# Kernel optimization log

Hardware: AMD Instinct MI355X
Metric: run time of the kernel (lower is better)

The kernel has to match this reference:

```python
import math
import jax, jax.numpy as jnp
import numpy as np

T, B, E, H = 2048, 1, 2048, 32
HD = E // H          # head_dim = 64
HALF = HD // 2       # rotary half = 32
SCALE_LENGTH = 1024


def duplicate_interleave(m):
    # [S, HALF] -> [S, HD], each column duplicated adjacently
    return jnp.repeat(m, 2, axis=-1)


def rotate_every_two(x):
    # x: [BH, S, HD]
    x1 = x[:, :, ::2]
    x2 = x[:, :, 1::2]
    return jnp.stack((-x2, x1), axis=-1).reshape(x.shape)


def apply_rotary_pos_emb(x, sin, cos, scale):
    # sin/cos/scale: [S, HALF]; x: [BH, S, HD]
    sin2 = duplicate_interleave(sin * scale)
    cos2 = duplicate_interleave(cos * scale)
    return x * cos2 + rotate_every_two(x) * sin2


def setup_inputs() -> dict:
    key = jax.random.key(0)
    ks = jax.random.split(key, 8)
    std = 0.02
    query = jax.random.normal(ks[0], (T, B, E), jnp.float32)
    key_t = jax.random.normal(ks[1], (T, B, E), jnp.float32)
    value = jax.random.normal(ks[2], (T, B, E), jnp.float32)
    Wq = jax.random.normal(ks[3], (E, E), jnp.float32) * std
    Wk = jax.random.normal(ks[4], (E, E), jnp.float32) * std
    Wv = jax.random.normal(ks[5], (E, E), jnp.float32) * std
    Wo = jax.random.normal(ks[6], (E, E), jnp.float32) * std
    bq = jnp.zeros((E,), jnp.float32)
    bk = jnp.zeros((E,), jnp.float32)
    bv = jnp.zeros((E,), jnp.float32)
    bo = jnp.zeros((E,), jnp.float32)
    # XPos-style rotary tables
    pos = jnp.arange(T, dtype=jnp.float32)
    inv_freq = 1.0 / (10000.0 ** (jnp.arange(HALF, dtype=jnp.float32) / HALF))
    ang = pos[:, None] * inv_freq[None, :]          # [T, HALF]
    sin = jnp.sin(ang)
    cos = jnp.cos(ang)
    scale_base = 512.0
    dim_scale = (jnp.arange(0, HD, 2, dtype=jnp.float32) + 0.4 * HD) / (1.4 * HD)
    xscale = dim_scale[None, :] ** (pos[:, None] / scale_base)  # [T, HALF]
    # causal additive mask
    attn_mask = jnp.where(jnp.triu(jnp.ones((T, T), bool), k=1), -1e9, 0.0).astype(jnp.float32)
    return {"query": query, "key": key_t, "value": value,
            "Wq": Wq, "bq": bq, "Wk": Wk, "bk": bk, "Wv": Wv, "bv": bv,
            "Wo": Wo, "bo": bo, "sin": sin, "cos": cos, "xscale": xscale,
            "attn_mask": attn_mask, "scale_length": SCALE_LENGTH}


def reference(query, key, value, Wq, bq, Wk, bk, Wv, bv, Wo, bo,
              sin, cos, xscale, attn_mask, scale_length):
    tgt_len, bsz, embed_dim = query.shape
    scaling = HD ** -0.5

    def proj(x, W, b):
        y = x @ W.T + b                                # [T, B, E]
        return y.reshape(tgt_len, bsz * H, HD).transpose(1, 0, 2)  # [BH, T, HD]

    q = proj(query, Wq, bq)
    k = proj(key, Wk, bk)
    v = proj(value, Wv, bv)

    # self-attention XPos rotary: k scaled by 1/xscale, q by xscale (last q_len rows)
    k = apply_rotary_pos_emb(k, sin, cos, 1.0 / xscale)
    q = apply_rotary_pos_emb(q, sin[-tgt_len:], cos[-tgt_len:], xscale[-tgt_len:])

    src_len = k.shape[1]
    if src_len > scale_length:
        pos_k = jnp.arange(src_len - tgt_len, src_len, dtype=jnp.float32)
        scale_attention = jnp.maximum(1.0, jnp.log(pos_k) / math.log(scale_length))
        q = q * scale_attention[None, :, None]

    q = q * scaling
    attn_weights = jnp.einsum('btd,bsd->bts', q, k)      # [BH, T, S]
    attn_weights = attn_weights + attn_mask[None, :, :]
    attn_weights = jax.nn.softmax(attn_weights.astype(jnp.float32), axis=-1
                                  ).astype(q.dtype)
    attn = jnp.einsum('bts,bsd->btd', attn_weights, v)   # [BH, T, HD]
    attn = attn.transpose(1, 0, 2).reshape(tgt_len, bsz, embed_dim)
    attn = attn @ Wo.T + bo
    return attn
```

## Files before the change

### kernel.cpp

```cpp
#include <hip/hip_runtime.h>
#include <hip/hip_bf16.h>
#include <math.h>

#define T_LEN 2048
#define EMB   2048
#define NH    32
#define HD    64
#define HALF  32

typedef __attribute__((ext_vector_type(8))) short short8v;
typedef __attribute__((ext_vector_type(4))) float floatx4;

__device__ inline void gload_lds16(const void* g, void* l) {
    __builtin_amdgcn_global_load_lds(
        (const __attribute__((address_space(1))) unsigned int*)g,
        (__attribute__((address_space(3))) unsigned int*)l,
        16, 0, 0);
}

__device__ inline ushort f2bf(float x) {
    union { float f; unsigned u; } c; c.f = x;
    const unsigned r = c.u + 0x7FFFu + ((c.u >> 16) & 1u);
    return (ushort)(r >> 16);
}

#define BARRIER() do { asm volatile("" ::: "memory"); \
    __builtin_amdgcn_s_barrier(); asm volatile("" ::: "memory"); } while (0)
#define VMW8() asm volatile("s_waitcnt vmcnt(8)" ::: "memory")
#define VMW0() asm volatile("s_waitcnt vmcnt(0)" ::: "memory")

__global__ __launch_bounds__(256) void conv_all(
    const float* __restrict__ s0, const float* __restrict__ s1,
    const float* __restrict__ s2, const float* __restrict__ s3,
    const float* __restrict__ s4, const float* __restrict__ s5,
    const float* __restrict__ s6, ushort* __restrict__ dst,
    const float* __restrict__ sinp, const float* __restrict__ cosp,
    const float* __restrict__ xscale,
    float2* __restrict__ qt, float2* __restrict__ kt)
{
    if (blockIdx.x >= 14336) {
        const int idx = (blockIdx.x - 14336) * 256 + threadIdx.x;
        const int t = idx >> 5;
        const float s = sinp[idx], c = cosp[idx], xs = xscale[idx];
        float sa = 1.f;
        if (t >= 2) {
            const float lv = __logf((float)t) * 0.14426950408889634f;
            sa = lv > 1.f ? lv : 1.f;
        }
        const float qs = xs * sa * 0.125f * 1.4426950408889634f;
        qt[idx] = make_float2(c * qs, s * qs);
        const float ks = 1.f / xs;
        kt[idx] = make_float2(c * ks, s * ks);
        return;
    }
    const int idx = blockIdx.x * 256 + threadIdx.x;
    const int t = idx >> 19;
    const int r = (idx & 524287) * 8;
    const float* in = t == 0 ? s0 : t == 1 ? s1 : t == 2 ? s2 : t == 3 ? s3
                    : t == 4 ? s4 : t == 5 ? s5 : s6;
    const float4 v0 = *reinterpret_cast<const float4*>(&in[r]);
    const float4 v1 = *reinterpret_cast<const float4*>(&in[r + 4]);
    ushort o[8];
    o[0] = f2bf(v0.x); o[1] = f2bf(v0.y); o[2] = f2bf(v0.z); o[3] = f2bf(v0.w);
    o[4] = f2bf(v1.x); o[5] = f2bf(v1.y); o[6] = f2bf(v1.z); o[7] = f2bf(v1.w);
    *reinterpret_cast<uint4*>(&dst[(size_t)t * 4194304 + r]) =
        *reinterpret_cast<const uint4*>(o);
}

#define QBM 256
#define QBN 256

#define STAGE_A3(tau, h, slot) do {                                            \
    const int _tc = (tau) * 64;                                                \
    _Pragma("unroll") for (int _i = 0; _i < 2; ++_i) {                         \
        gload_lds16(&Ap[(size_t)(bm + (h) * 128 + wid * 16 + _i * 8 + rl) * 2048 + _tc + csw], \
                    &lds[(slot) * 16384 + (h) * 8192 + (wid * 16 + _i * 8) * 64]); \
    } } while (0)

#define STAGE_B2(tau, h, slot) do {                                            \
    const int _tc = (tau) * 64;                                                \
    _Pragma("unroll") for (int _i = 0; _i < 2; ++_i) {                         \
        gload_lds16(&Bp[(size_t)(bn + (h) * 128 + wid * 16 + _i * 8 + rl) * 2048 + _tc + csw], \
                    &lds[49152 + (slot) * 16384 + (h) * 8192 + (wid * 16 + _i * 8) * 64]); \
    } } while (0)

#define PH(sa_, sb_, mp, VMWSTMT, ...) do {                                    \
    if ((mp) == 0) {                                                           \
        _Pragma("unroll") for (int n = 0; n < 4; ++n) {                        \
            bf[n][0] = ldB(sb_, n, 0);                                         \
            bf[n][1] = ldB(sb_, n, 1);                                         \
        }                                                                      \
    }                                                                          \
    af[0][0] = ldA(sa_, (mp) * 2, 0);     af[0][1] = ldA(sa_, (mp) * 2, 1);    \
    af[1][0] = ldA(sa_, (mp) * 2 + 1, 0); af[1][1] = ldA(sa_, (mp) * 2 + 1, 1);\
    __VA_ARGS__;                                                               \
    BARRIER();                                                                 \
    __builtin_amdgcn_s_setprio(1);                                             \
    _Pragma("unroll") for (int mm = 0; mm < 2; ++mm)                           \
    _Pragma("unroll") for (int n = 0; n < 4; ++n)                              \
    _Pragma("unroll") for (int kk = 0; kk < 2; ++kk)                           \
        acc[(mp) * 2 + mm][n] = __builtin_amdgcn_mfma_f32_16x16x32_bf16(       \
            af[mm][kk], bf[n][kk], acc[(mp) * 2 + mm][n], 0, 0, 0);            \
    __builtin_amdgcn_s_setprio(0);                                             \
    VMWSTMT;                                                                   \
    BARRIER();                                                                 \
} while (0)

#define TILE6(sa, sb, sa2, tau2, LASTVMW) do {                                 \
    PH(sa, sb, 0, (void)0, STAGE_A3(tau2, 0, sa2));                            \
    PH(sa, sb, 1, (void)0, STAGE_A3(tau2, 1, sa2));                            \
    PH(sa, sb, 2, (void)0, STAGE_B2(tau2, 0, sb));                             \
    PH(sa, sb, 3, LASTVMW, STAGE_B2(tau2, 1, sb));                             \
} while (0)

__global__ __launch_bounds__(512, 2) void gemm_qkv8(
    const ushort* __restrict__ Astack,
    const ushort* __restrict__ Wstack,
    const float* __restrict__ bq, const float* __restrict__ bk,
    const float* __restrict__ bv,
    ushort* __restrict__ outQ, ushort* __restrict__ outK,
    ushort* __restrict__ outVt,
    const float2* __restrict__ qtab, const float2* __restrict__ ktab)
{
    __shared__ ushort lds[81920];
    const int tid  = threadIdx.x;
    const int lane = tid & 63;
    const int wid  = tid >> 6;

    const int b   = blockIdx.x + blockIdx.y * 24;
    const int xcd = b & 7;
    const int idx = b >> 3;
    const int bx  = xcd * 3 + (idx >> 3);
    const int by  = idx & 7;
    const int which = bx >> 3;
    const int bn  = (bx & 7) * QBN;
    const int bm  = by * QBM;
    const ushort* Ap = Astack + (size_t)which * 4194304;
    const ushort* Bp = Wstack + (size_t)which * 4194304;

    const int rl  = lane >> 3;
    const int csw = (((lane & 7) ^ ((lane >> 3) & 7)) * 8);
    const int lm  = lane & 15;
    const int lg  = lane >> 4;
    const char* ldsb = reinterpret_cast<const char*>(lds);

    auto ldA = [&](int slot, int m, int kk) -> short8v {
        const int row = m * 16 + lm;
        const int off = (slot * 16384 + (wid >> 2) * 8192) * 2 + row * 128
                      + (((kk * 4 + lg) ^ (row & 7)) * 16);
        return *reinterpret_cast<const short8v*>(ldsb + off);
    };
    auto ldB = [&](int slot, int n, int kk) -> short8v {
        const int row = (wid & 1) * 64 + n * 16 + lm;
        const int off = (49152 + slot * 16384 + ((wid & 3) >> 1) * 8192) * 2
                      + row * 128 + (((kk * 4 + lg) ^ (row & 7)) * 16);
        return *reinterpret_cast<const short8v*>(ldsb + off);
    };

    floatx4 acc[8][4] = {};
    short8v bf[4][2];
    short8v af[2][2];

    STAGE_A3(0, 0, 0); STAGE_A3(0, 1, 0);
    STAGE_B2(0, 0, 0); STAGE_B2(0, 1, 0);
    STAGE_A3(1, 0, 1); STAGE_A3(1, 1, 1);
    STAGE_B2(1, 0, 1); STAGE_B2(1, 1, 1);
    VMW8();
    BARRIER();

    for (int i = 0; i < 5; ++i) {
        const int t = 6 * i;
        TILE6(0, 0, 2, t + 2, VMW8());
        TILE6(1, 1, 0, t + 3, VMW8());
        TILE6(2, 0, 1, t + 4, VMW8());
        TILE6(0, 1, 2, t + 5, VMW8());
        TILE6(1, 0, 0, t + 6, VMW8());
        TILE6(2, 1, 1, t + 7, VMW8());
    }
    PH(0, 0, 0, (void)0, (void)0);
    PH(0, 0, 1, (void)0, (void)0);
    PH(0, 0, 2, (void)0, (void)0);
    PH(0, 0, 3, VMW0(),  (void)0);
    PH(1, 1, 0, (void)0, (void)0);
    PH(1, 1, 1, (void)0, (void)0);
    PH(1, 1, 2, (void)0, (void)0);
    PH(1, 1, 3, (void)0, (void)0);

    const float* bias = which == 0 ? bq : which == 1 ? bk : bv;
    const float2* tbl = which == 0 ? qtab : ktab;
    #pragma unroll
    for (int m = 0; m < 8; ++m) {
        #pragma unroll
        for (int n = 0; n < 4; ++n) {
            const int col = bn + (wid & 3) * 64 + n * 16 + lm;
            const float bz = bias[col];
            const int row0 = bm + (wid >> 2) * 128 + m * 16 + lg * 4;
            if (which == 2) {
                ushort o4[4];
                #pragma unroll
                for (int j = 0; j < 4; ++j)
                    o4[j] = f2bf(acc[m][n][j] + bz);
                *reinterpret_cast<uint2*>(&outVt[(size_t)col * T_LEN + row0]) =
                    *reinterpret_cast<const uint2*>(o4);
            } else {
                ushort* O = which == 0 ? outQ : outK;
                const int p = (col & 63) >> 1;
                const bool even = (col & 1) == 0;
                #pragma unroll
                for (int j = 0; j < 4; ++j) {
                    const int row = row0 + j;
                    const float v = acc[m][n][j] + bz;
                    const float pv = __shfl_xor(v, 1);
                    const float2 cs = tbl[row * HALF + p];
                    const float outv = even ? v * cs.x - pv * cs.y
                                            : v * cs.x + pv * cs.y;
                    O[(size_t)row * EMB + col] = f2bf(outv);
                }
            }
        }
    }
}

#define GBM 128
#define GBN 128
#define GBK 64

__global__ __launch_bounds__(256) void gemm_out_sk(
    const ushort* __restrict__ A,
    const ushort* __restrict__ B,
    ushort* __restrict__ P)
{
    __shared__ ushort As[GBM * GBK];
    __shared__ ushort Bs[GBN * GBK];
    const int tid  = threadIdx.x;
    const int lane = tid & 63;
    const int wid  = tid >> 6;
    const int bm = blockIdx.y * GBM;
    const int bn = blockIdx.x * GBN;
    const int z  = blockIdx.z;
    const int wr = (wid >> 1) * 64;
    const int wc = (wid & 1) * 64;

    floatx4 acc[4][4] = {};

    const int lrow  = lane >> 3;
    const int lcolb = (lane & 7) * 8;

    for (int k0 = z * 1024; k0 < (z + 1) * 1024; k0 += GBK) {
        #pragma unroll
        for (int c = 0; c < 4; ++c) {
            const int chunk = wid * 4 + c;
            const int row = chunk * 8 + lrow;
            gload_lds16(&A[(size_t)(bm + row) * EMB + k0 + lcolb], &As[chunk * 512]);
            gload_lds16(&B[(size_t)(bn + row) * EMB + k0 + lcolb], &Bs[chunk * 512]);
        }
        __syncthreads();
        #pragma unroll
        for (int kk = 0; kk < 2; ++kk) {
            short8v a[4], b[4];
            #pragma unroll
            for (int m = 0; m < 4; ++m)
                a[m] = *reinterpret_cast<const short8v*>(
                    &As[(wr + m * 16 + (lane & 15)) * GBK + kk * 32 + (lane >> 4) * 8]);
            #pragma unroll
            for (int n = 0; n < 4; ++n)
                b[n] = *reinterpret_cast<const short8v*>(
                    &Bs[(wc + n * 16 + (lane & 15)) * GBK + kk * 32 + (lane >> 4) * 8]);
            #pragma unroll
            for (int m = 0; m < 4; ++m)
                #pragma unroll
                for (int n = 0; n < 4; ++n)
                    acc[m][n] = __builtin_amdgcn_mfma_f32_16x16x32_bf16(
                        a[m], b[n], acc[m][n], 0, 0, 0);
        }
        __syncthreads();
    }

    ushort* Pz = P + (size_t)z * 4194304;
    const int cr = (lane >> 4) * 4;
    const int cc = lane & 15;
    #pragma unroll
    for (int m = 0; m < 4; ++m) {
        #pragma unroll
        for (int n = 0; n < 4; ++n) {
            const int col = bn + wc + n * 16 + cc;
            #pragma unroll
            for (int j = 0; j < 4; ++j) {
                const int row = bm + wr + m * 16 + cr + j;
                Pz[(size_t)row * EMB + col] = f2bf(acc[m][n][j]);
            }
        }
    }
}

__global__ __launch_bounds__(256) void reduce_out(
    const ushort* __restrict__ P, const float* __restrict__ bias,
    float* __restrict__ C)
{
    const int i = (blockIdx.x * 256 + threadIdx.x) * 8;
    const uint4 pa = *reinterpret_cast<const uint4*>(&P[i]);
    const uint4 pb = *reinterpret_cast<const uint4*>(&P[4194304 + i]);
    const ushort* ua = reinterpret_cast<const ushort*>(&pa);
    const ushort* ub = reinterpret_cast<const ushort*>(&pb);
    const int cb = i & 2047;
    float o[8];
    #pragma unroll
    for (int j = 0; j < 8; ++j) {
        union { unsigned u; float f; } fa, fb;
        fa.u = (unsigned)ua[j] << 16;
        fb.u = (unsigned)ub[j] << 16;
        o[j] = fa.f + fb.f + bias[cb + j];
    }
    *reinterpret_cast<float4*>(&C[i])     = make_float4(o[0], o[1], o[2], o[3]);
    *reinterpret_cast<float4*>(&C[i + 4]) = make_float4(o[4], o[5], o[6], o[7]);
}

__global__ __launch_bounds__(256) void flash_attn_mfma(
    const ushort* __restrict__ Qb,
    const ushort* __restrict__ Kb,
    const ushort* __restrict__ Vt,
    ushort* __restrict__ Ob)
{
    __shared__ ushort Ks[2][64 * 64];
    __shared__ ushort Vs[2][64 * 64];
    __shared__ ushort Ps[4][16 * 64];

    const int h   = blockIdx.x;
    const int qb  = (T_LEN / 64 - 1) - blockIdx.y;
    const int tid = threadIdx.x;
    const int lane = tid & 63;
    const int wid  = tid >> 6;
    const int qrow_w = qb * 64 + wid * 16;
    const int lm = lane & 15;
    const int lg = lane >> 4;

    short8v qf[2];
    {
        const ushort* qp = &Qb[(size_t)(qrow_w + lm) * EMB + h * HD + lg * 8];
        qf[0] = *reinterpret_cast<const short8v*>(qp);
        qf[1] = *reinterpret_cast<const short8v*>(qp + 32);
    }

    floatx4 oacc[4] = {};
    float m = -1e30f, l = 0.f;

    const int srow = lane >> 3;
    const int schk = lane & 7;

    {
        #pragma unroll
        for (int i = 0; i < 2; ++i) {
            const int slot = wid * 2 + i;
            const int row  = slot * 8 + srow;
            const int cswz = (schk ^ (row & 7)) * 8;
            gload_lds16(&Kb[(size_t)row * EMB + h * HD + cswz], &Ks[0][slot * 512]);
            gload_lds16(&Vt[(size_t)(h * HD + row) * T_LEN + cswz], &Vs[0][slot * 512]);
        }
    }
    __syncthreads();

    for (int kb = 0; kb <= qb; ++kb) {
        const int cur = kb & 1;
        if (kb < qb) {
            const int nkb = kb + 1;
            #pragma unroll
            for (int i = 0; i < 2; ++i) {
                const int slot = wid * 2 + i;
                const int row  = slot * 8 + srow;
                const int cswz = (schk ^ (row & 7)) * 8;
                gload_lds16(&Kb[(size_t)(nkb * 64 + row) * EMB + h * HD + cswz],
                            &Ks[cur ^ 1][slot * 512]);
                gload_lds16(&Vt[(size_t)(h * HD + row) * T_LEN + nkb * 64 + cswz],
                            &Vs[cur ^ 1][slot * 512]);
            }
        }

        float sv[16];
        __builtin_amdgcn_s_setprio(1);
        #pragma unroll
        for (int t = 0; t < 4; ++t) {
            floatx4 sacc = {};
            const int srow_l = t * 16 + lm;
            const char* krow = reinterpret_cast<const char*>(Ks[cur]) + srow_l * 128;
            const int swz = (srow_l & 7) << 4;
            #pragma unroll
            for (int kk = 0; kk < 2; ++kk) {
                const int cb = (kk * 64 + lg * 16) ^ swz;
                short8v kf = *reinterpret_cast<const short8v*>(krow + cb);
                sacc = __builtin_amdgcn_mfma_f32_16x16x32_bf16(kf, qf[kk], sacc, 0, 0, 0);
            }
            sv[t * 4 + 0] = sacc[0]; sv[t * 4 + 1] = sacc[1];
            sv[t * 4 + 2] = sacc[2]; sv[t * 4 + 3] = sacc[3];
        }
        __builtin_amdgcn_s_setprio(0);

        const int qg = qrow_w + lm;
        if (kb == qb) {
            #pragma unroll
            for (int t = 0; t < 4; ++t)
                #pragma unroll
                for (int r = 0; r < 4; ++r) {
                    const int sg = kb * 64 + t * 16 + lg * 4 + r;
                    if (sg > qg) sv[t * 4 + r] = -1e30f;
                }
        }

        const float mx0 = fmaxf(fmaxf(fmaxf(sv[0], sv[1]), fmaxf(sv[2], sv[3])),
                                fmaxf(fmaxf(sv[4], sv[5]), fmaxf(sv[6], sv[7])));
        const float mx1 = fmaxf(fmaxf(fmaxf(sv[8], sv[9]), fmaxf(sv[10], sv[11])),
                                fmaxf(fmaxf(sv[12], sv[13]), fmaxf(sv[14], sv[15])));
        float mx = fmaxf(mx0, mx1);
        mx = fmaxf(mx, __shfl_xor(mx, 16));
        mx = fmaxf(mx, __shfl_xor(mx, 32));
        float corr = 1.f;
        if (!__all(mx - m <= 11.544f)) {
            const float mnew = fmaxf(m, mx);
            corr = exp2f(m - mnew);
            m = mnew;
            float corr4[4];
            #pragma unroll
            for (int r = 0; r < 4; ++r)
                corr4[r] = __shfl(corr, lg * 4 + r);
            #pragma unroll
            for (int td = 0; td < 4; ++td)
                #pragma unroll
                for (int r = 0; r < 4; ++r)
                    oacc[td][r] *= corr4[r];
        }
        float psum[8];
        unsigned pw[8];
        #pragma unroll
        for (int i = 0; i < 8; ++i) {
            const float p0 = exp2f(sv[2 * i + 0] - m);
            const float p1 = exp2f(sv[2 * i + 1] - m);
            psum[i] = p0 + p1;
            const __hip_bfloat162 h2 = __float22bfloat162_rn(make_float2(p0, p1));
            pw[i] = *reinterpret_cast<const unsigned*>(&h2);
        }
        float ps = ((psum[0] + psum[1]) + (psum[2] + psum[3]))
                 + ((psum[4] + psum[5]) + (psum[6] + psum[7]));
        ps += __shfl_xor(ps, 16);
        ps += __shfl_xor(ps, 32);
        l = l * corr + ps;

        {
            char* pbase = reinterpret_cast<char*>(&Ps[wid][0]) + lm * 128;
            const int swz = (lm & 7) << 4;
            #pragma unroll
            for (int t = 0; t < 4; ++t) {
                uint2 w;
                w.x = pw[2 * t + 0];
                w.y = pw[2 * t + 1];
                const int cb = (t * 32 + lg * 8) ^ swz;
                *reinterpret_cast<uint2*>(pbase + cb) = w;
            }
        }

        const char* pwave = reinterpret_cast<const char*>(&Ps[wid][0]);
        __builtin_amdgcn_s_setprio(1);
        #pragma unroll
        for (int kk = 0; kk < 2; ++kk) {
            const int acb = (kk * 64 + lg * 16) ^ ((lm & 7) << 4);
            short8v pa = *reinterpret_cast<const short8v*>(pwave + lm * 128 + acb);
            #pragma unroll
            for (int td = 0; td < 4; ++td) {
                const int d = td * 16 + lm;
                const int bcb = (kk * 64 + lg * 16) ^ ((d & 7) << 4);
                short8v vb = *reinterpret_cast<const short8v*>(
                    reinterpret_cast<const char*>(Vs[cur]) + d * 128 + bcb);
                oacc[td] = __builtin_amdgcn_mfma_f32_16x16x32_bf16(pa, vb, oacc[td], 0, 0, 0);
            }
        }
        __builtin_amdgcn_s_setprio(0);

        __syncthreads();
    }

    float invl[4];
    #pragma unroll
    for (int r = 0; r < 4; ++r)
        invl[r] = 1.f / __shfl(l, lg * 4 + r);
    #pragma unroll
    for (int td = 0; td < 4; ++td) {
        #pragma unroll
        for (int r = 0; r < 4; ++r) {
            const int trow = qrow_w + lg * 4 + r;
            const int col  = h * HD + td * 16 + lm;
            Ob[(size_t)trow * EMB + col] = f2bf(oacc[td][r] * invl[r]);
        }
    }
}

extern "C" void kernel_launch(void* const* d_in, const int* in_sizes, int n_in,
                              void* d_out, int out_size, void* d_ws, size_t ws_size,
                              hipStream_t stream) {
    const float* query = (const float*)d_in[0];
    const float* key   = (const float*)d_in[1];
    const float* value = (const float*)d_in[2];
    const float* Wq = (const float*)d_in[3];
    const float* bq = (const float*)d_in[4];
    const float* Wk = (const float*)d_in[5];
    const float* bk = (const float*)d_in[6];
    const float* Wv = (const float*)d_in[7];
    const float* bv = (const float*)d_in[8];
    const float* Wo = (const float*)d_in[9];
    const float* bo = (const float*)d_in[10];
    const float* sinp   = (const float*)d_in[11];
    const float* cosp   = (const float*)d_in[12];
    const float* xscale = (const float*)d_in[13];
    float* out = (float*)d_out;

    const size_t MB = 1024 * 1024;
    char* ws = (char*)d_ws;
    ushort* bWqkv = (ushort*)(ws + 0 * MB);
    ushort* bWo   = (ushort*)(ws + 24 * MB);
    ushort* bAqkv = (ushort*)(ws + 32 * MB);
    ushort* bQ  = (ushort*)(ws + 56 * MB);
    ushort* bK  = (ushort*)(ws + 64 * MB);
    ushort* bVt = (ushort*)(ws + 72 * MB);
    ushort* bAo = (ushort*)(ws + 80 * MB);
    float2* qtab = (float2*)(ws + 88 * MB);
    float2* ktab = (float2*)(ws + 88 * MB + 512 * 1024);
    ushort* Pout = (ushort*)(ws + 32 * MB);

    conv_all<<<14336 + 256, 256, 0, stream>>>(
        Wq, Wk, Wv, Wo, query, key, value, bWqkv,
        sinp, cosp, xscale, qtab, ktab);

    dim3 gQKV(24, 8);
    gemm_qkv8<<<gQKV, 512, 0, stream>>>(bAqkv, bWqkv, bq, bk, bv,
                                        bQ, bK, bVt, qtab, ktab);

    dim3 gFlash(NH, T_LEN / 64);
    flash_attn_mfma<<<gFlash, 256, 0, stream>>>(bQ, bK, bVt, bAo);

    dim3 gOut(EMB / GBN, T_LEN / GBM, 2);
    gemm_out_sk<<<gOut, 256, 0, stream>>>(bAo, bWo, Pout);
    reduce_out<<<T_LEN * EMB / (256 * 8), 256, 0, stream>>>(Pout, bo, out);
}
```

Before: 171.6 us.

## Rewrite flash attention with 32x32 MFMA and 128-row query tiles

The flash attention kernel now uses 32x32x16 bf16 MFMA instead of 16x16x32, with each wave owning 32 query rows and each block 128 rows. Each K/V tile loaded into LDS is therefore reused by twice as many query rows, halving the grid. The P matrix is now passed between lanes with cross-half shuffles instead of an LDS round trip, and tiles lying entirely above the causal diagonal are skipped per wave. The cost is higher register pressure, fewer blocks for occupancy and load balance, and more per-lane shuffle work.

```diff
diff --git a/kernel.cpp b/kernel.cpp
--- a/kernel.cpp
+++ b/kernel.cpp
@@ -10,6 +10,7 @@
 
 typedef __attribute__((ext_vector_type(8))) short short8v;
 typedef __attribute__((ext_vector_type(4))) float floatx4;
+typedef __attribute__((ext_vector_type(16))) float floatx16;
 
 __device__ inline void gload_lds16(const void* g, void* l) {
     __builtin_amdgcn_global_load_lds(
@@ -315,7 +316,7 @@
     *reinterpret_cast<float4*>(&C[i + 4]) = make_float4(o[4], o[5], o[6], o[7]);
 }
 
-__global__ __launch_bounds__(256) void flash_attn_mfma(
+__global__ __launch_bounds__(256) void flash_attn_mfma32(
     const ushort* __restrict__ Qb,
     const ushort* __restrict__ Kb,
     const ushort* __restrict__ Vt,
@@ -323,171 +324,162 @@
 {
     __shared__ ushort Ks[2][64 * 64];
     __shared__ ushort Vs[2][64 * 64];
-    __shared__ ushort Ps[4][16 * 64];
 
     const int h   = blockIdx.x;
-    const int qb  = (T_LEN / 64 - 1) - blockIdx.y;
+    const int qb  = (T_LEN / 128 - 1) - blockIdx.y;
     const int tid = threadIdx.x;
     const int lane = tid & 63;
     const int wid  = tid >> 6;
-    const int qrow_w = qb * 64 + wid * 16;
-    const int lm = lane & 15;
-    const int lg = lane >> 4;
-
-    short8v qf[2];
+    const int qrow_w = qb * 128 + wid * 32;
+    const int lq = lane & 31;
+    const int hh = lane >> 5;
+
+    short8v qf[4];
     {
-        const ushort* qp = &Qb[(size_t)(qrow_w + lm) * EMB + h * HD + lg * 8];
+        const ushort* qp = &Qb[(size_t)(qrow_w + lq) * EMB + h * HD + hh * 8];
         qf[0] = *reinterpret_cast<const short8v*>(qp);
-        qf[1] = *reinterpret_cast<const short8v*>(qp + 32);
-    }
-
-    floatx4 oacc[4] = {};
+        qf[1] = *reinterpret_cast<const short8v*>(qp + 16);
+        qf[2] = *reinterpret_cast<const short8v*>(qp + 32);
+        qf[3] = *reinterpret_cast<const short8v*>(qp + 48);
+    }
+
+    floatx16 oacc[2] = {};
     float m = -1e30f, l = 0.f;
 
     const int srow = lane >> 3;
     const int schk = lane & 7;
-
-    {
-        #pragma unroll
-        for (int i = 0; i < 2; ++i) {
-            const int slot = wid * 2 + i;
-            const int row  = slot * 8 + srow;
-            const int cswz = (schk ^ (row & 7)) * 8;
-            gload_lds16(&Kb[(size_t)row * EMB + h * HD + cswz], &Ks[0][slot * 512]);
-            gload_lds16(&Vt[(size_t)(h * HD + row) * T_LEN + cswz], &Vs[0][slot * 512]);
-        }
+    const int nkb = 2 * qb + 2;
+
+    #pragma unroll
+    for (int i = 0; i < 2; ++i) {
+        const int slot = wid * 2 + i;
+        const int row  = slot * 8 + srow;
+        const int cswz = (schk ^ (row & 7)) * 8;
+        gload_lds16(&Kb[(size_t)row * EMB + h * HD + cswz], &Ks[0][slot * 512]);
+        gload_lds16(&Vt[(size_t)(h * HD + row) * T_LEN + cswz], &Vs[0][slot * 512]);
     }
     __syncthreads();
 
-    for (int kb = 0; kb <= qb; ++kb) {
+    for (int kb = 0; kb < nkb; ++kb) {
         const int cur = kb & 1;
-        if (kb < qb) {
-            const int nkb = kb + 1;
+        if (kb + 1 < nkb) {
+            const int nk = kb + 1;
             #pragma unroll
             for (int i = 0; i < 2; ++i) {
                 const int slot = wid * 2 + i;
                 const int row  = slot * 8 + srow;
                 const int cswz = (schk ^ (row & 7)) * 8;
-                gload_lds16(&Kb[(size_t)(nkb * 64 + row) * EMB + h * HD + cswz],
+                gload_lds16(&Kb[(size_t)(nk * 64 + row) * EMB + h * HD + cswz],
                             &Ks[cur ^ 1][slot * 512]);
-                gload_lds16(&Vt[(size_t)(h * HD + row) * T_LEN + nkb * 64 + cswz],
+                gload_lds16(&Vt[(size_t)(h * HD + row) * T_LEN + nk * 64 + cswz],
                             &Vs[cur ^ 1][slot * 512]);
             }
         }
 
-        float sv[16];
-        __builtin_amdgcn_s_setprio(1);
-        #pragma unroll
-        for (int t = 0; t < 4; ++t) {
-            floatx4 sacc = {};
-            const int srow_l = t * 16 + lm;
-            const char* krow = reinterpret_cast<const char*>(Ks[cur]) + srow_l * 128;
-            const int swz = (srow_l & 7) << 4;
-            #pragma unroll
-            for (int kk = 0; kk < 2; ++kk) {
-                const int cb = (kk * 64 + lg * 16) ^ swz;
-                short8v kf = *reinterpret_cast<const short8v*>(krow + cb);
-                sacc = __builtin_amdgcn_mfma_f32_16x16x32_bf16(kf, qf[kk], sacc, 0, 0, 0);
-            }
-            sv[t * 4 + 0] = sacc[0]; sv[t * 4 + 1] = sacc[1];
-            sv[t * 4 + 2] = sacc[2]; sv[t * 4 + 3] = sacc[3];
-        }
-        __builtin_amdgcn_s_setprio(0);
-
-        const int qg = qrow_w + lm;
-        if (kb == qb) {
-            #pragma unroll
-            for (int t = 0; t < 4; ++t)
-                #pragma unroll
-                for (int r = 0; r < 4; ++r) {
-                    const int sg = kb * 64 + t * 16 + lg * 4 + r;
-                    if (sg > qg) sv[t * 4 + r] = -1e30f;
+        if (kb * 64 <= qrow_w + 31) {
+            const bool diag = (kb * 64 + 63 > qrow_w);
+
+            floatx16 sacc[2] = {};
+            __builtin_amdgcn_s_setprio(1);
+            #pragma unroll
+            for (int st = 0; st < 2; ++st) {
+                const int srow_l = st * 32 + lq;
+                const char* krow = reinterpret_cast<const char*>(Ks[cur])
+                                 + srow_l * 128;
+                const int swz = srow_l & 7;
+                #pragma unroll
+                for (int c = 0; c < 4; ++c) {
+                    short8v kf = *reinterpret_cast<const short8v*>(
+                        krow + (((2 * c + hh) ^ swz) * 16));
+                    sacc[st] = __builtin_amdgcn_mfma_f32_32x32x16_bf16(
+                        kf, qf[c], sacc[st], 0, 0, 0);
                 }
-        }
-
-        const float mx0 = fmaxf(fmaxf(fmaxf(sv[0], sv[1]), fmaxf(sv[2], sv[3])),
-                                fmaxf(fmaxf(sv[4], sv[5]), fmaxf(sv[6], sv[7])));
-        const float mx1 = fmaxf(fmaxf(fmaxf(sv[8], sv[9]), fmaxf(sv[10], sv[11])),
-                                fmaxf(fmaxf(sv[12], sv[13]), fmaxf(sv[14], sv[15])));
-        float mx = fmaxf(mx0, mx1);
-        mx = fmaxf(mx, __shfl_xor(mx, 16));
-        mx = fmaxf(mx, __shfl_xor(mx, 32));
-        float corr = 1.f;
-        if (!__all(mx - m <= 11.544f)) {
-            const float mnew = fmaxf(m, mx);
-            corr = exp2f(m - mnew);
-            m = mnew;
-            float corr4[4];
-            #pragma unroll
-            for (int r = 0; r < 4; ++r)
-                corr4[r] = __shfl(corr, lg * 4 + r);
-            #pragma unroll
-            for (int td = 0; td < 4; ++td)
-                #pragma unroll
-                for (int r = 0; r < 4; ++r)
-                    oacc[td][r] *= corr4[r];
-        }
-        float psum[8];
-        unsigned pw[8];
-        #pragma unroll
-        for (int i = 0; i < 8; ++i) {
-            const float p0 = exp2f(sv[2 * i + 0] - m);
-            const float p1 = exp2f(sv[2 * i + 1] - m);
-            psum[i] = p0 + p1;
-            const __hip_bfloat162 h2 = __float22bfloat162_rn(make_float2(p0, p1));
-            pw[i] = *reinterpret_cast<const unsigned*>(&h2);
-        }
-        float ps = ((psum[0] + psum[1]) + (psum[2] + psum[3]))
-                 + ((psum[4] + psum[5]) + (psum[6] + psum[7]));
-        ps += __shfl_xor(ps, 16);
-        ps += __shfl_xor(ps, 32);
-        l = l * corr + ps;
-
-        {
-            char* pbase = reinterpret_cast<char*>(&Ps[wid][0]) + lm * 128;
-            const int swz = (lm & 7) << 4;
-            #pragma unroll
-            for (int t = 0; t < 4; ++t) {
-                uint2 w;
-                w.x = pw[2 * t + 0];
-                w.y = pw[2 * t + 1];
-                const int cb = (t * 32 + lg * 8) ^ swz;
-                *reinterpret_cast<uint2*>(pbase + cb) = w;
-            }
-        }
-
-        const char* pwave = reinterpret_cast<const char*>(&Ps[wid][0]);
-        __builtin_amdgcn_s_setprio(1);
-        #pragma unroll
-        for (int kk = 0; kk < 2; ++kk) {
-            const int acb = (kk * 64 + lg * 16) ^ ((lm & 7) << 4);
-            short8v pa = *reinterpret_cast<const short8v*>(pwave + lm * 128 + acb);
-            #pragma unroll
-            for (int td = 0; td < 4; ++td) {
-                const int d = td * 16 + lm;
-                const int bcb = (kk * 64 + lg * 16) ^ ((d & 7) << 4);
-                short8v vb = *reinterpret_cast<const short8v*>(
-                    reinterpret_cast<const char*>(Vs[cur]) + d * 128 + bcb);
-                oacc[td] = __builtin_amdgcn_mfma_f32_16x16x32_bf16(pa, vb, oacc[td], 0, 0, 0);
-            }
-        }
-        __builtin_amdgcn_s_setprio(0);
+            }
+            __builtin_amdgcn_s_setprio(0);
+
+            float sv[32];
+            const int qg = qrow_w + lq;
+            #pragma unroll
+            for (int st = 0; st < 2; ++st)
+                #pragma unroll
+                for (int r = 0; r < 16; ++r) {
+                    float v = sacc[st][r];
+                    if (diag) {
+                        const int sg = kb * 64 + st * 32 + (r & 3) + 8 * (r >> 2) + 4 * hh;
+                        if (sg > qg) v = -1e30f;
+                    }
+                    sv[st * 16 + r] = v;
+                }
+
+            float mx = sv[0];
+            #pragma unroll
+            for (int i = 1; i < 32; ++i) mx = fmaxf(mx, sv[i]);
+            mx = fmaxf(mx, __shfl_xor(mx, 32));
+
+            float corr = 1.f;
+            if (!__all(mx - m <= 11.544f)) {
+                const float mnew = fmaxf(m, mx);
+                corr = exp2f(m - mnew);
+                m = mnew;
+                #pragma unroll
+                for (int r = 0; r < 16; ++r) {
+                    const float cr = __shfl(corr, (r & 3) + 8 * (r >> 2) + 4 * hh);
+                    oacc[0][r] *= cr;
+                    oacc[1][r] *= cr;
+                }
+            }
+
+            float ps = 0.f;
+            unsigned w[16];
+            #pragma unroll
+            for (int i = 0; i < 16; ++i) {
+                const float p0 = exp2f(sv[2 * i + 0] - m);
+                const float p1 = exp2f(sv[2 * i + 1] - m);
+                ps += p0 + p1;
+                const __hip_bfloat162 h2 = __float22bfloat162_rn(make_float2(p0, p1));
+                w[i] = *reinterpret_cast<const unsigned*>(&h2);
+            }
+            ps += __shfl_xor(ps, 32);
+            l = l * corr + ps;
+
+            unsigned px[16];
+            #pragma unroll
+            for (int i = 0; i < 16; ++i)
+                px[i] = (unsigned)__shfl_xor((int)w[i], 32);
+
+            __builtin_amdgcn_s_setprio(1);
+            #pragma unroll
+            for (int c = 0; c < 4; ++c) {
+                const int b4 = (c >> 1) * 8 + (c & 1) * 4;
+                unsigned aw[4];
+                aw[0] = hh ? px[b4 + 2] : w[b4 + 0];
+                aw[1] = hh ? px[b4 + 3] : w[b4 + 1];
+                aw[2] = hh ? w[b4 + 2] : px[b4 + 0];
+                aw[3] = hh ? w[b4 + 3] : px[b4 + 1];
+                short8v pa = *reinterpret_cast<const short8v*>(aw);
+                #pragma unroll
+                for (int dt = 0; dt < 2; ++dt) {
+                    const int d = dt * 32 + lq;
+                    short8v vb = *reinterpret_cast<const short8v*>(
+                        reinterpret_cast<const char*>(Vs[cur]) + d * 128
+                        + (((2 * c + hh) ^ (d & 7)) * 16));
+                    oacc[dt] = __builtin_amdgcn_mfma_f32_32x32x16_bf16(
+                        pa, vb, oacc[dt], 0, 0, 0);
+                }
+            }
+            __builtin_amdgcn_s_setprio(0);
+        }
 
         __syncthreads();
     }
 
-    float invl[4];
     #pragma unroll
-    for (int r = 0; r < 4; ++r)
-        invl[r] = 1.f / __shfl(l, lg * 4 + r);
-    #pragma unroll
-    for (int td = 0; td < 4; ++td) {
-        #pragma unroll
-        for (int r = 0; r < 4; ++r) {
-            const int trow = qrow_w + lg * 4 + r;
-            const int col  = h * HD + td * 16 + lm;
-            Ob[(size_t)trow * EMB + col] = f2bf(oacc[td][r] * invl[r]);
-        }
+    for (int r = 0; r < 16; ++r) {
+        const int qr = (r & 3) + 8 * (r >> 2) + 4 * hh;
+        const float invl = 1.f / __shfl(l, qr);
+        const size_t rowoff = (size_t)(qrow_w + qr) * EMB + h * HD;
+        Ob[rowoff + lq]      = f2bf(oacc[0][r] * invl);
+        Ob[rowoff + 32 + lq] = f2bf(oacc[1][r] * invl);
     }
 }
 
@@ -531,8 +523,8 @@
     gemm_qkv8<<<gQKV, 512, 0, stream>>>(bAqkv, bWqkv, bq, bk, bv,
                                         bQ, bK, bVt, qtab, ktab);
 
-    dim3 gFlash(NH, T_LEN / 64);
-    flash_attn_mfma<<<gFlash, 256, 0, stream>>>(bQ, bK, bVt, bAo);
+    dim3 gFlash(NH, T_LEN / 128);
+    flash_attn_mfma32<<<gFlash, 256, 0, stream>>>(bQ, bK, bVt, bAo);
 
     dim3 gOut(EMB / GBN, T_LEN / GBM, 2);
     gemm_out_sk<<<gOut, 256, 0, stream>>>(bAo, bWo, Pout);
```

New measurement: 203.6 us. +18.7%, slower.
